# Kernel optimization log

Hardware: AMD Instinct MI355X
Metric: run time of the kernel (lower is better)

## Reference

```python
import jax, jax.numpy as jnp
import numpy as np

N_NODES = 10000
N_EDGES = 160000
D = 42          # node_input_dim == node_hidden_dim
DE = 10         # edge_input_dim
DEH = 42        # edge_hidden_dim
N_STEPS = 6


def setup_inputs() -> dict:
    key = jax.random.key(0)
    ks = jax.random.split(key, 16)
    s = 0.1
    return {
        "n_feat": jax.random.normal(ks[0], (N_NODES, D), jnp.float32),
        "e_feat": jax.random.normal(ks[1], (N_EDGES, DE), jnp.float32),
        "src": jax.random.randint(ks[2], (N_EDGES,), 0, N_NODES),
        "dst": jax.random.randint(ks[3], (N_EDGES,), 0, N_NODES),
        # lin0: node_input_dim -> node_hidden_dim
        "lin0_w": s * jax.random.normal(ks[4], (D, D), jnp.float32),
        "lin0_b": s * jax.random.normal(ks[5], (D,), jnp.float32),
        # message_layer: hidden -> hidden
        "msg_w": s * jax.random.normal(ks[6], (D, D), jnp.float32),
        "msg_b": s * jax.random.normal(ks[7], (D,), jnp.float32),
        # edge_network: Linear(10,42) -> ReLU -> Linear(42, 42*42)
        "en_w1": s * jax.random.normal(ks[8], (DE, DEH), jnp.float32),
        "en_b1": s * jax.random.normal(ks[9], (DEH,), jnp.float32),
        "en_w2": s * jax.random.normal(ks[10], (DEH, D * D), jnp.float32),
        "en_b2": s * jax.random.normal(ks[11], (D * D,), jnp.float32),
        # NNConv bias (DGL NNConv has bias=True by default)
        "conv_b": s * jax.random.normal(ks[12], (D,), jnp.float32),
    }


def reference(n_feat, e_feat, src, dst,
              lin0_w, lin0_b, msg_w, msg_b,
              en_w1, en_b1, en_w2, en_b2, conv_b):
    N, d = n_feat.shape
    init = n_feat
    out = jax.nn.relu(n_feat @ lin0_w + lin0_b)                      # [N, d]
    # Per-edge weight matrices from edge features (e_feat is constant
    # across steps, so the edge MLP is hoisted out of the loop).
    w_edge = (jax.nn.relu(e_feat @ en_w1 + en_b1) @ en_w2 + en_b2)   # [E, d*d]
    w_edge = w_edge.reshape(-1, d, d)                                # [E, d_in, d_out]
    for _ in range(N_STEPS):
        # NNConv: gather src feats, per-edge matvec, scatter-sum to dst
        msgs = jnp.einsum('ei,eio->eo', out[src], w_edge)            # [E, d]
        agg = jax.ops.segment_sum(msgs, dst, num_segments=N)         # [N, d]
        # residual (in==out -> identity res_fc) + bias, then outer ReLU
        m = jax.nn.relu(agg + out + conv_b)
        out = jax.nn.relu(m @ msg_w + msg_b)
    return out + init
```

## Files before the change

### kernel.cpp

```cpp
#include <hip/hip_runtime.h>
#include <hip/hip_bf16.h>


#define N_NODES 10000
#define N_EDGES 160000
#define NCHK 5000
#define D 42
#define DE 10
#define XSTR 48
#define KI 1806
#define NKSTEP 57
#define SSTR 1832

typedef __attribute__((ext_vector_type(8))) short short8;
typedef __attribute__((ext_vector_type(4))) float f32x4;

__global__ __launch_bounds__(256) void k_lin0(const float* __restrict__ nf,
        const float* __restrict__ w, const float* __restrict__ b,
        __hip_bfloat16* __restrict__ out16) {
    int idx = blockIdx.x * 256 + threadIdx.x;
    if (idx >= N_NODES * XSTR) return;
    int n = idx / XSTR, j = idx % XSTR;
    float v = 0.f;
    if (j < D) {
        const float* row = nf + n * D;
        float acc = b[j];
        #pragma unroll
        for (int i = 0; i < D; ++i) acc = fmaf(row[i], w[i * D + j], acc);
        v = fmaxf(acc, 0.f);
    }
    out16[idx] = __float2bfloat16(v);
}

__global__ __launch_bounds__(256) void k_T2B(const float* __restrict__ w2,
        const float* __restrict__ b2, __hip_bfloat16* __restrict__ Bfr) {
    int idx = blockIdx.x * 256 + threadIdx.x;
    if (idx >= 3 * NKSTEP * 64 * 8) return;
    int j = idx & 7, lane = (idx >> 3) & 63;
    int ks = (idx >> 9) % NKSTEP, nt = idx / (NKSTEP * 512);
    int col = nt * 16 + (lane & 15);
    int k = ks * 32 + ((lane >> 4) * 8) + j;
    float v = 0.f;
    if (col < D && k < KI) {
        int kk = k / D, ii = k % D;
        v = (kk < D) ? w2[kk * (D * D) + ii * D + col] : b2[ii * D + col];
    }
    Bfr[idx] = __float2bfloat16(v);
}

__global__ __launch_bounds__(256) void k_hist(const int* __restrict__ dst,
        int* __restrict__ cnt) {
    int e = blockIdx.x * 256 + threadIdx.x;
    if (e < N_EDGES) atomicAdd(&cnt[dst[e]], 1);
}

__global__ __launch_bounds__(1024) void k_scan(const int* __restrict__ cnt,
        int* __restrict__ row_ptr, int* __restrict__ cursor) {
    __shared__ int buf[1024];
    __shared__ int s_run;
    const int t = threadIdx.x;
    if (t == 0) s_run = 0;
    __syncthreads();
    for (int base = 0; base < N_NODES; base += 1024) {
        int v = (base + t < N_NODES) ? cnt[base + t] : 0;
        buf[t] = v;
        __syncthreads();
        for (int off = 1; off < 1024; off <<= 1) {
            int add = (t >= off) ? buf[t - off] : 0;
            __syncthreads();
            buf[t] += add;
            __syncthreads();
        }
        int excl = buf[t] - v;
        if (base + t < N_NODES) {
            int val = s_run + excl;
            row_ptr[base + t] = val;
            cursor[base + t]  = val;
        }
        __syncthreads();
        if (t == 0) s_run += buf[1023];
        __syncthreads();
    }
    if (t == 0) { row_ptr[N_NODES] = s_run; cursor[N_NODES] = s_run; }
}

__global__ __launch_bounds__(256) void k_scatter(const int* __restrict__ dst,
        const int* __restrict__ src, int* __restrict__ cursor,
        int* __restrict__ srcp, int* __restrict__ eperm) {
    int e = blockIdx.x * 256 + threadIdx.x;
    if (e < N_EDGES) {
        int p = atomicAdd(&cursor[dst[e]], 1);
        srcp[p] = src[e];
        eperm[p] = e;
    }
}

__global__ __launch_bounds__(256) void k_hT(const float* __restrict__ ef,
        const float* __restrict__ w1, const float* __restrict__ b1,
        const int* __restrict__ eperm, __hip_bfloat16* __restrict__ hpT) {
    const int c = blockIdx.x;
    const int t = threadIdx.x;
    for (int j = t; j < 48 * 32; j += 256) {
        int k = j >> 5, ep = j & 31;
        int e = eperm[c * 32 + ep];
        float v;
        if (k < D) {
            const float* row = ef + (size_t)e * DE;
            float acc = b1[k];
            #pragma unroll
            for (int i = 0; i < DE; ++i) acc = fmaf(row[i], w1[i * D + k], acc);
            v = fmaxf(acc, 0.f);
        } else {
            v = (k == D) ? 1.0f : 0.f;
        }
        hpT[(size_t)c * 1536 + j] = __float2bfloat16(v);
    }
}

__global__ __launch_bounds__(256) void k_gx(
        const __hip_bfloat16* __restrict__ x16, const int* __restrict__ srcp,
        __hip_bfloat16* __restrict__ xeT) {
    __shared__ short sx[128][50];
    const int t = threadIdx.x;
    const int base = blockIdx.x * 128;
    const short* xs = (const short*)x16;
    for (int idx = t; idx < 128 * 6; idx += 256) {
        int el = idx / 6, cs = idx % 6;
        int sp = srcp[base + el];
        *(short8*)&sx[el][cs * 8] = *(const short8*)(xs + (size_t)sp * XSTR + cs * 8);
    }
    __syncthreads();
    short* out = (short*)xeT + (size_t)blockIdx.x * 4 * 1536;
    for (int idx = t; idx < 768; idx += 256) {
        int cc = idx / 192, rem = idx % 192, row = rem >> 2, h8 = rem & 3;
        short8 v;
        #pragma unroll
        for (int j = 0; j < 8; ++j) v[j] = sx[cc * 32 + h8 * 8 + j][row];
        *(short8*)(out + (size_t)cc * 1536 + row * 32 + h8 * 8) = v;
    }
}

#define MFMA(A, B, C) C = __builtin_amdgcn_mfma_f32_16x16x32_bf16(A, B, C, 0, 0, 0)

__global__ __launch_bounds__(512, 5) void k_step7(
        const __hip_bfloat16* __restrict__ hpT,
        const __hip_bfloat16* __restrict__ xeT,
        const __hip_bfloat16* __restrict__ out_in,
        const int* __restrict__ row_ptr,
        const __hip_bfloat16* __restrict__ Bfr,
        const float* __restrict__ nf, const float* __restrict__ msg_w,
        const float* __restrict__ msg_b, const float* __restrict__ conv_b,
        __hip_bfloat16* __restrict__ out16_dst, float* __restrict__ fout,
        int last) {
    __shared__ __align__(16) __hip_bfloat16 sS[8 * SSTR];
    __shared__ float sR[8 * 48];
    __shared__ float sM[8 * 48];
    const int t = threadIdx.x;
    const int wv = t >> 6;
    const int l = t & 63;
    const int g = l >> 4;
    const int g8 = g * 8;
    const int cl = l & 15;
    const int n0 = blockIdx.x * 8;
    const short* hpTs = (const short*)hpT;
    const short* xeTs = (const short*)xeT;

    for (int i = t; i < 8 * 48; i += 512) sR[i] = 0.f;
    for (int i = t; i < 8 * 18; i += 512)
        sS[(i / 18) * SSTR + KI + (i % 18)] = __float2bfloat16(0.f);

    {
        const int node = n0 + wv;
        const int beg = row_ptr[node], end = row_ptr[node + 1];
        const int c0 = beg >> 5;
        const int nc = (end > beg) ? ((end - 1) >> 5) - c0 + 1 : 0;

        f32x4 cc[9];
        #pragma unroll
        for (int i = 0; i < 9; ++i) cc[i] = {0.f, 0.f, 0.f, 0.f};

        for (int ci = 0; ci < nc; ++ci) {
            const int c = c0 + ci;
            const int c32 = c << 5;
            const size_t hb = (size_t)c * 1536 + cl * 32 + g8;
            short8 a0 = *(const short8*)(hpTs + hb);
            short8 a1 = *(const short8*)(hpTs + hb + 512);
            short8 a2 = *(const short8*)(hpTs + hb + 1024);
            short8 b0 = *(const short8*)(xeTs + hb);
            short8 b1 = *(const short8*)(xeTs + hb + 512);
            short8 b2 = *(const short8*)(xeTs + hb + 1024);
            if (c32 < beg || c32 + 32 > end) {
                #pragma unroll
                for (int j = 0; j < 8; ++j) {
                    int ep = c32 + g8 + j;
                    if (ep < beg || ep >= end) { a0[j] = 0; a1[j] = 0; a2[j] = 0; }
                }
            }
            MFMA(a0, b0, cc[0]); MFMA(a0, b1, cc[1]); MFMA(a0, b2, cc[2]);
            MFMA(a1, b0, cc[3]); MFMA(a1, b1, cc[4]); MFMA(a1, b2, cc[5]);
            MFMA(a2, b0, cc[6]); MFMA(a2, b1, cc[7]); MFMA(a2, b2, cc[8]);
        }
        #define ST(CI, MT, NT)                                               \
            _Pragma("unroll")                                                \
            for (int r = 0; r < 4; ++r) {                                    \
                int m = (MT) * 16 + g * 4 + r;                               \
                int col = (NT) * 16 + cl;                                    \
                if (m < 43 && col < D)                                       \
                    sS[wv * SSTR + m * D + col] = __float2bfloat16(cc[CI][r]); \
            }
        ST(0, 0, 0) ST(1, 0, 1) ST(2, 0, 2)
        ST(3, 1, 0) ST(4, 1, 1) ST(5, 1, 2)
        ST(6, 2, 0) ST(7, 2, 1) ST(8, 2, 2)
        #undef ST
    }
    __syncthreads();

    {
        const int ks0 = (wv == 0) ? 0 : (wv * 7 + 1);
        const int ks1 = wv * 7 + 8;
        f32x4 d0 = {0.f, 0.f, 0.f, 0.f}, d1 = d0, d2 = d0;
        const short* sSrow = (const short*)sS + (cl & 7) * SSTR + g8;
        const short* bb = (const short*)Bfr + (size_t)l * 8;
        for (int ks = ks0; ks < ks1; ++ks) {
            short8 a  = *(const short8*)(sSrow + ks * 32);
            short8 B0 = *(const short8*)(bb + (size_t)(0 * NKSTEP + ks) * 512);
            short8 B1 = *(const short8*)(bb + (size_t)(1 * NKSTEP + ks) * 512);
            short8 B2 = *(const short8*)(bb + (size_t)(2 * NKSTEP + ks) * 512);
            MFMA(a, B0, d0); MFMA(a, B1, d1); MFMA(a, B2, d2);
        }
        if (g < 2) {
            const int rl = g * 4;
            #pragma unroll
            for (int r = 0; r < 4; ++r) {
                atomicAdd(&sR[(rl + r) * 48 + cl],      d0[r]);
                atomicAdd(&sR[(rl + r) * 48 + 16 + cl], d1[r]);
                atomicAdd(&sR[(rl + r) * 48 + 32 + cl], d2[r]);
            }
        }
    }
    __syncthreads();

    float* sW = (float*)sS;
    for (int i = t; i < D * D; i += 512) sW[i] = msg_w[i];
    for (int idx = t; idx < 8 * 48; idx += 512) {
        int nl_ = idx / 48, o = idx % 48;
        float mv = 0.f;
        if (o < D) {
            float res = __bfloat162float(out_in[(size_t)(n0 + nl_) * XSTR + o]);
            mv = fmaxf(sR[idx] + res + conv_b[o], 0.f);
        }
        sM[idx] = mv;
    }
    __syncthreads();

    for (int idx = t; idx < 8 * 48; idx += 512) {
        int nl_ = idx / 48, pcol = idx % 48;
        if (pcol < D) {
            float s = msg_b[pcol];
            #pragma unroll 6
            for (int o = 0; o < D; ++o)
                s = fmaf(sM[nl_ * 48 + o], sW[o * D + pcol], s);
            float v = fmaxf(s, 0.f);
            if (last) {
                fout[(size_t)(n0 + nl_) * D + pcol] =
                    v + nf[(size_t)(n0 + nl_) * D + pcol];
            } else {
                out16_dst[(size_t)(n0 + nl_) * XSTR + pcol] = __float2bfloat16(v);
            }
        } else if (!last) {
            out16_dst[(size_t)(n0 + nl_) * XSTR + pcol] = __float2bfloat16(0.f);
        }
    }
}

extern "C" void kernel_launch(void* const* d_in, const int* in_sizes, int n_in,
                              void* d_out, int out_size, void* d_ws, size_t ws_size,
                              hipStream_t stream) {
    const float* nf    = (const float*)d_in[0];
    const float* ef    = (const float*)d_in[1];
    const int*   src   = (const int*)d_in[2];
    const int*   dst   = (const int*)d_in[3];
    const float* lin0w = (const float*)d_in[4];
    const float* lin0b = (const float*)d_in[5];
    const float* msgw  = (const float*)d_in[6];
    const float* msgb  = (const float*)d_in[7];
    const float* enw1  = (const float*)d_in[8];
    const float* enb1  = (const float*)d_in[9];
    const float* enw2  = (const float*)d_in[10];
    const float* enb2  = (const float*)d_in[11];
    const float* convb = (const float*)d_in[12];

    char* p = (char*)d_ws;
    auto alloc = [&](size_t bytes) -> char* {
        char* r = p; p += (bytes + 255) & ~(size_t)255; return r;
    };
    __hip_bfloat16* outA = (__hip_bfloat16*)alloc((size_t)N_NODES * XSTR * 2);
    __hip_bfloat16* outB = (__hip_bfloat16*)alloc((size_t)N_NODES * XSTR * 2);
    __hip_bfloat16* hpT  = (__hip_bfloat16*)alloc((size_t)NCHK * 1536 * 2);
    __hip_bfloat16* xeT  = (__hip_bfloat16*)alloc((size_t)NCHK * 1536 * 2);
    __hip_bfloat16* Bfr  = (__hip_bfloat16*)alloc((size_t)3 * NKSTEP * 64 * 8 * 2);
    int* cnt    = (int*)alloc((N_NODES + 1) * 4);
    int* rowp   = (int*)alloc((N_NODES + 1) * 4);
    int* cur    = (int*)alloc((N_NODES + 1) * 4);
    int* srcp   = (int*)alloc((size_t)N_EDGES * 4);
    int* eperm  = (int*)alloc((size_t)N_EDGES * 4);

    hipMemsetAsync(cnt, 0, (N_NODES + 1) * 4, stream);
    k_lin0<<<(N_NODES * XSTR + 255) / 256, 256, 0, stream>>>(nf, lin0w, lin0b, outA);
    k_T2B<<<(3 * NKSTEP * 64 * 8 + 255) / 256, 256, 0, stream>>>(enw2, enb2, Bfr);
    k_hist<<<(N_EDGES + 255) / 256, 256, 0, stream>>>(dst, cnt);
    k_scan<<<1, 1024, 0, stream>>>(cnt, rowp, cur);
    k_scatter<<<(N_EDGES + 255) / 256, 256, 0, stream>>>(dst, src, cur, srcp, eperm);
    k_hT<<<NCHK, 256, 0, stream>>>(ef, enw1, enb1, eperm, hpT);

    const int tiles = N_NODES / 8;
    __hip_bfloat16* bufs[2] = {outA, outB};
    for (int s_i = 0; s_i < 6; ++s_i) {
        const __hip_bfloat16* cin = bufs[s_i % 2];
        __hip_bfloat16* cout = bufs[(s_i + 1) % 2];
        int last = (s_i == 5) ? 1 : 0;
        k_gx<<<NCHK / 4, 256, 0, stream>>>(cin, srcp, xeT);
        k_step7<<<tiles, 512, 0, stream>>>(hpT, xeT, cin, rowp, Bfr,
                                           nf, msgw, msgb, convb,
                                           cout, (float*)d_out, last);
    }
}
```

Baseline: 373.5 us.

## Split per-node edge-MFMA tiles across two waves with 1024-thread blocks

Doubles the block to 1024 threads so that two waves share each node's 3x3 grid of edge-reduction MFMA tiles, five tiles on one and four on the other, instead of one wave doing all nine. The second GEMM's 57 k-steps are spread over 16 waves instead of 8. This halves the per-wave accumulator registers and the serial MFMA chain for high-degree nodes. In exchange, each xeT B fragment is loaded twice (once per half), the hpT row fetched by both halves is duplicated, and the larger block needs every wave resident at once, which constrains scheduling.

```diff
diff --git a/kernel.cpp b/kernel.cpp
--- a/kernel.cpp
+++ b/kernel.cpp
@@ -142,7 +142,7 @@
 
 #define MFMA(A, B, C) C = __builtin_amdgcn_mfma_f32_16x16x32_bf16(A, B, C, 0, 0, 0)
 
-__global__ __launch_bounds__(512, 5) void k_step7(
+__global__ __launch_bounds__(1024, 8) void k_step8(
         const __hip_bfloat16* __restrict__ hpT,
         const __hip_bfloat16* __restrict__ xeT,
         const __hip_bfloat16* __restrict__ out_in,
@@ -165,40 +165,51 @@
     const short* hpTs = (const short*)hpT;
     const short* xeTs = (const short*)xeT;
 
-    for (int i = t; i < 8 * 48; i += 512) sR[i] = 0.f;
-    for (int i = t; i < 8 * 18; i += 512)
+    for (int i = t; i < 8 * 48; i += 1024) sR[i] = 0.f;
+    for (int i = t; i < 8 * 18; i += 1024)
         sS[(i / 18) * SSTR + KI + (i % 18)] = __float2bfloat16(0.f);
 
     {
-        const int node = n0 + wv;
+        const int nl = wv >> 1;
+        const int half = wv & 1;
+        const int node = n0 + nl;
         const int beg = row_ptr[node], end = row_ptr[node + 1];
         const int c0 = beg >> 5;
         const int nc = (end > beg) ? ((end - 1) >> 5) - c0 + 1 : 0;
 
-        f32x4 cc[9];
+        f32x4 cc[5];
         #pragma unroll
-        for (int i = 0; i < 9; ++i) cc[i] = {0.f, 0.f, 0.f, 0.f};
+        for (int i = 0; i < 5; ++i) cc[i] = {0.f, 0.f, 0.f, 0.f};
 
         for (int ci = 0; ci < nc; ++ci) {
             const int c = c0 + ci;
             const int c32 = c << 5;
             const size_t hb = (size_t)c * 1536 + cl * 32 + g8;
-            short8 a0 = *(const short8*)(hpTs + hb);
-            short8 a1 = *(const short8*)(hpTs + hb + 512);
-            short8 a2 = *(const short8*)(hpTs + hb + 1024);
             short8 b0 = *(const short8*)(xeTs + hb);
             short8 b1 = *(const short8*)(xeTs + hb + 512);
             short8 b2 = *(const short8*)(xeTs + hb + 1024);
+            short8 aX, aY;
+            if (half == 0) {
+                aX = *(const short8*)(hpTs + hb);
+                aY = *(const short8*)(hpTs + hb + 512);
+            } else {
+                aX = *(const short8*)(hpTs + hb + 512);
+                aY = *(const short8*)(hpTs + hb + 1024);
+            }
             if (c32 < beg || c32 + 32 > end) {
                 #pragma unroll
                 for (int j = 0; j < 8; ++j) {
                     int ep = c32 + g8 + j;
-                    if (ep < beg || ep >= end) { a0[j] = 0; a1[j] = 0; a2[j] = 0; }
+                    if (ep < beg || ep >= end) { aX[j] = 0; aY[j] = 0; }
                 }
             }
-            MFMA(a0, b0, cc[0]); MFMA(a0, b1, cc[1]); MFMA(a0, b2, cc[2]);
-            MFMA(a1, b0, cc[3]); MFMA(a1, b1, cc[4]); MFMA(a1, b2, cc[5]);
-            MFMA(a2, b0, cc[6]); MFMA(a2, b1, cc[7]); MFMA(a2, b2, cc[8]);
+            if (half == 0) {
+                MFMA(aX, b0, cc[0]); MFMA(aX, b1, cc[1]); MFMA(aX, b2, cc[2]);
+                MFMA(aY, b0, cc[3]); MFMA(aY, b1, cc[4]);
+            } else {
+                MFMA(aX, b2, cc[0]);
+                MFMA(aY, b0, cc[1]); MFMA(aY, b1, cc[2]); MFMA(aY, b2, cc[3]);
+            }
         }
         #define ST(CI, MT, NT)                                               \
             _Pragma("unroll")                                                \
@@ -206,18 +217,20 @@
                 int m = (MT) * 16 + g * 4 + r;                               \
                 int col = (NT) * 16 + cl;                                    \
                 if (m < 43 && col < D)                                       \
-                    sS[wv * SSTR + m * D + col] = __float2bfloat16(cc[CI][r]); \
-            }
-        ST(0, 0, 0) ST(1, 0, 1) ST(2, 0, 2)
-        ST(3, 1, 0) ST(4, 1, 1) ST(5, 1, 2)
-        ST(6, 2, 0) ST(7, 2, 1) ST(8, 2, 2)
+                    sS[nl * SSTR + m * D + col] = __float2bfloat16(cc[CI][r]); \
+            }
+        if (half == 0) {
+            ST(0, 0, 0) ST(1, 0, 1) ST(2, 0, 2) ST(3, 1, 0) ST(4, 1, 1)
+        } else {
+            ST(0, 1, 2) ST(1, 2, 0) ST(2, 2, 1) ST(3, 2, 2)
+        }
         #undef ST
     }
     __syncthreads();
 
     {
-        const int ks0 = (wv == 0) ? 0 : (wv * 7 + 1);
-        const int ks1 = wv * 7 + 8;
+        const int ks0 = (wv * NKSTEP) >> 4;
+        const int ks1 = ((wv + 1) * NKSTEP) >> 4;
         f32x4 d0 = {0.f, 0.f, 0.f, 0.f}, d1 = d0, d2 = d0;
         const short* sSrow = (const short*)sS + (cl & 7) * SSTR + g8;
         const short* bb = (const short*)Bfr + (size_t)l * 8;
@@ -241,8 +254,8 @@
     __syncthreads();
 
     float* sW = (float*)sS;
-    for (int i = t; i < D * D; i += 512) sW[i] = msg_w[i];
-    for (int idx = t; idx < 8 * 48; idx += 512) {
+    for (int i = t; i < D * D; i += 1024) sW[i] = msg_w[i];
+    for (int idx = t; idx < 8 * 48; idx += 1024) {
         int nl_ = idx / 48, o = idx % 48;
         float mv = 0.f;
         if (o < D) {
@@ -253,7 +266,7 @@
     }
     __syncthreads();
 
-    for (int idx = t; idx < 8 * 48; idx += 512) {
+    for (int idx = t; idx < 8 * 48; idx += 1024) {
         int nl_ = idx / 48, pcol = idx % 48;
         if (pcol < D) {
             float s = msg_b[pcol];
@@ -320,8 +333,8 @@
         __hip_bfloat16* cout = bufs[(s_i + 1) % 2];
         int last = (s_i == 5) ? 1 : 0;
         k_gx<<<NCHK / 4, 256, 0, stream>>>(cin, srcp, xeT);
-        k_step7<<<tiles, 512, 0, stream>>>(hpT, xeT, cin, rowp, Bfr,
-                                           nf, msgw, msgb, convb,
-                                           cout, (float*)d_out, last);
-    }
-}
+        k_step8<<<tiles, 1024, 0, stream>>>(hpT, xeT, cin, rowp, Bfr,
+                                            nf, msgw, msgb, convb,
+                                            cout, (float*)d_out, last);
+    }
+}
```

Measured after the change: 500.5 us. 1.34x slower.
